# Kernel optimization log

Measured on AMD Instinct MI355X. Metric: run time of the kernel, lower is better.

## Reference

```python
import jax, jax.numpy as jnp
import numpy as np

B, I, H, NC, T = 128, 256, 512, 16, 24
M = 14            # max ACT ticks (forward default M=14)
EPS = 0.01        # eps_halting default


def setup_inputs() -> dict:
    key = jax.random.key(0)
    ks = jax.random.split(key, 9)
    s = 1.0 / np.sqrt(H).astype(np.float32)
    u = lambda k, shape: jax.random.uniform(k, shape, jnp.float32, -s, s)
    return {
        "x": jax.random.normal(ks[0], (B, I, T), jnp.float32),
        # LSTMCell params, torch gate order (i, f, g, o)
        "W_ih": u(ks[1], (4 * H, I)),
        "W_hh": u(ks[2], (4 * H, H)),
        "b_ih": u(ks[3], (4 * H,)),
        "b_hh": u(ks[4], (4 * H,)),
        "halt_w": u(ks[5], (1, H)),
        "halt_b": u(ks[6], (1,)),
        "dec_w": u(ks[7], (NC, H)),
        "dec_b": u(ks[8], (NC,)),
    }


def _forward(x, W_ih, W_hh, b_ih, b_hh, halt_w, halt_b, dec_w, dec_b):
    Bn = x.shape[0]
    Hn = W_hh.shape[1]

    def lstm_cell(xi, h, c):
        g = xi @ W_ih.T + b_ih + h @ W_hh.T + b_hh
        i, f, gg, o = jnp.split(g, 4, axis=-1)
        c = jax.nn.sigmoid(f) * c + jax.nn.sigmoid(i) * jnp.tanh(gg)
        h = jax.nn.sigmoid(o) * jnp.tanh(c)
        return h, c

    def act_step(carry, xi):
        # Run M ticks; ACT weighting (ph) zeroes contributions past the halt step,
        # exactly reproducing the torch early-exit semantics.
        def tick(sc, _):
            h, c = lstm_cell(xi, sc[0], sc[1])
            pn = jax.nn.sigmoid(h @ halt_w.T + halt_b)[:, 0]  # [B]
            y = h @ dec_w.T + dec_b                            # [B, NC]
            return (h, c), (pn, h, c, y)

        _, (p_hist, s_hist, c_hist, y_hist) = jax.lax.scan(tick, carry, None, length=M)
        # p_hist [M,B]; s/c_hist [M,B,H]; y_hist [M,B,NC]
        pt_cum = jnp.cumsum(p_hist, axis=0)                    # [M,B]
        all_halted = jnp.all(pt_cum >= 1.0 - EPS, axis=1)      # [M]
        n_stop = jnp.where(jnp.any(all_halted), jnp.argmax(all_halted) + 1, M)
        idx = jnp.arange(M)[:, None]
        # torch: p_max = min(1, cumsum); p_max[:, -1] = 1.0 (last executed tick)
        p_max = jnp.where(idx >= n_stop - 1, 1.0, jnp.minimum(1.0, pt_cum))
        ph = jnp.concatenate([p_max[:1], jnp.diff(p_max, axis=0)], axis=0)  # [M,B]
        st = jnp.einsum('mb,mbh->bh', ph, s_hist)
        ct = jnp.einsum('mb,mbh->bh', ph, c_hist)
        yt = jnp.einsum('mb,mbc->bc', ph, y_hist)
        nt = jnp.argmax(p_max, axis=0)                         # [B] first tick hitting 1.0
        rt = 1.0 - p_max[nt - 1, jnp.arange(Bn)]               # negative index wraps like torch
        pt = nt.astype(x.dtype) + rt
        return (st, ct), (yt, pt, nt)

    z = jnp.zeros((Bn, Hn), x.dtype)
    _, (Y, P, N) = jax.lax.scan(act_step, (z, z), jnp.moveaxis(x, -1, 0))
    Y = jnp.moveaxis(Y, 0, -1)     # [B, NC, T]
    P = jnp.sum(P, axis=0)         # [B]
    N = N.T                        # [B, T]
    return Y, P, N


def reference(x, W_ih, W_hh, b_ih, b_hh, halt_w, halt_b, dec_w, dec_b):
    return _forward(x, W_ih, W_hh, b_ih, b_hh, halt_w, halt_b, dec_w, dec_b)
```

## Files before the change

kernel.cpp:

```cpp
#include <hip/hip_runtime.h>
#include <math.h>

#define NWG 256
#define TPB 1024

static constexpr int Bc=128, Ic=256, Hc=512, NCc=16, Tc=24, Mc=14;
static constexpr int Y_SZ  = Bc*NCc*Tc;
static constexpr int P_OFF = Y_SZ;
static constexpr int N_OFF = Y_SZ + Bc;

static constexpr int HSZ    = Hc*Bc;
static constexpr int HB_OFF = 0;
static constexpr int SC_OFF = 2*HSZ;
static constexpr int HP_OFF = 4*HSZ;
static constexpr int DP_OFF = HP_OFF + 2*2048;

typedef float f4v __attribute__((ext_vector_type(4)));

__device__ __align__(64) unsigned g_bcnt[16][16];
__device__ __align__(64) unsigned g_bgen[16][16];
__device__ __align__(64) unsigned g_brc[16];
__device__ __align__(64) unsigned g_brg[16];

__device__ __forceinline__ float sigm(float v){ return 1.0f/(1.0f+expf(-v)); }

__device__ __forceinline__ void gstore(float* p, float v){
  __hip_atomic_store(p, v, __ATOMIC_RELAXED, __HIP_MEMORY_SCOPE_SYSTEM);
}
__device__ __forceinline__ float gload(const float* p){
  return *(const volatile float*)p;
}

__device__ __forceinline__ void gsync(int w){
  __syncthreads();
  if (threadIdx.x == 0) {
    asm volatile("" ::: "memory");
    const int g = w >> 4;
    unsigned prev = __hip_atomic_fetch_add(&g_bcnt[g][0], 1u, __ATOMIC_RELAXED, __HIP_MEMORY_SCOPE_SYSTEM);
    unsigned ep   = prev >> 4;
    if ((prev & 15u) == 15u) {
      unsigned rprev = __hip_atomic_fetch_add(&g_brc[0], 1u, __ATOMIC_RELAXED, __HIP_MEMORY_SCOPE_SYSTEM);
      if ((rprev & 15u) == 15u) {
        __hip_atomic_store(&g_brg[0], (rprev >> 4) + 1u, __ATOMIC_RELEASE, __HIP_MEMORY_SCOPE_SYSTEM);
      } else {
        while ((int)(__hip_atomic_load(&g_brg[0], __ATOMIC_RELAXED, __HIP_MEMORY_SCOPE_SYSTEM) - (ep + 1u)) < 0)
          __builtin_amdgcn_s_sleep(1);
      }
      __hip_atomic_store(&g_bgen[g][0], ep + 1u, __ATOMIC_RELEASE, __HIP_MEMORY_SCOPE_SYSTEM);
    } else {
      while ((int)(__hip_atomic_load(&g_bgen[g][0], __ATOMIC_RELAXED, __HIP_MEMORY_SCOPE_SYSTEM) - (ep + 1u)) < 0)
        __builtin_amdgcn_s_sleep(1);
    }
    asm volatile("" ::: "memory");
  }
  __syncthreads();
}

__global__ __launch_bounds__(TPB, 1) void act_lstm_kernel(
    const float* __restrict__ x,   const float* __restrict__ Wih,
    const float* __restrict__ Whh, const float* __restrict__ bih,
    const float* __restrict__ bhh, const float* __restrict__ hw,
    const float* __restrict__ hbp, const float* __restrict__ dw,
    const float* __restrict__ db,  float* __restrict__ out,
    float* __restrict__ ws)
{
  const int w    = blockIdx.x;
  const int tid  = threadIdx.x;
  const int lane = tid & 63;
  const int wid  = __builtin_amdgcn_readfirstlane(tid >> 6);
  const int bg   = w >> 4;
  const int js   = w & 15;
  const int kg   = wid;
  const int rl0  = lane, rl1 = lane + 64;
  const int grow0 = ((rl0>>5)<<9) + js*32 + (rl0&31);
  const int grow1 = ((rl1>>5)<<9) + js*32 + (rl1&31);
  const bool iscell = (tid < 256);
  const int jloc = tid >> 3, bl = tid & 7;
  const int jglob = js*32 + jloc;
  const int bglob = bg*8 + bl;

  float* hbuf = ws + HB_OFF;
  float* stc  = ws + SC_OFF;
  float* hpp  = ws + HP_OFF;
  float* decp = ws + DP_OFF;

  __shared__ float h_lds[4096];
  __shared__ float x_lds[2048];
  __shared__ float part[128*129];
  __shared__ float sums[1024];
  __shared__ float dp[4096];
  __shared__ float hp[256];
  __shared__ float pmh[128];
  __shared__ unsigned ldsu[2];

  const f4v* Wh0 = (const f4v*)(Whh + grow0*Hc) + kg*8;
  const f4v* Wh1 = (const f4v*)(Whh + grow1*Hc) + kg*8;
  const f4v* Wx0 = (const f4v*)(Wih + grow0*Ic) + kg*4;
  const f4v* Wx1 = (const f4v*)(Wih + grow1*Ic) + kg*4;

  float bsum[4] = {0,0,0,0};
  float hwj = 0.f;
  if (iscell) {
    #pragma unroll
    for (int g=0; g<4; ++g) bsum[g] = bih[g*512 + jglob] + bhh[g*512 + jglob];
    hwj = hw[jglob];
  }
  const float hb0 = hbp[0];

  float c = 0.f, st_run = 0.f, ct_run = 0.f, prev_pm = 0.f;
  float cumw=0.f, prevw=0.f, ntfw=0.f, rtvw=0.f, psumw=0.f;
  bool  ntsetw = false;
  int   gt = 0, lastpar = 0, pend_t = -1, pend_par = 0;
  float xg[4] = {0,0,0,0};

  for (int t = 0; t < Tc; ++t) {
    for (int mm = 0;; ++mm) {
      const bool do_h = !(mm == 0 && t == 0);
      float xv0 = 0.f, xv1 = 0.f;
      if (mm == 0) {
        const int i0 = tid >> 3, b0 = tid & 7;
        const int xb = (bg*8 + b0) * (Ic*Tc);
        xv0 = x[xb + i0*Tc + t];
        xv1 = x[xb + (i0+128)*Tc + t];
      }
      if (do_h) {
        const float* src = (mm == 0) ? (stc + lastpar*HSZ) : (hbuf + ((gt-1)&1)*HSZ);
        const int j = tid >> 1, q = tid & 1;
        f4v hv = *(const volatile f4v*)(src + j*128 + bg*8 + q*4);
        *(f4v*)&h_lds[tid*4] = hv;
      }
      __syncthreads();

      if (mm == 0) {
        x_lds[tid]        = xv0;
        x_lds[tid + 1024] = xv1;
        __syncthreads();
        float a0[8] = {0,0,0,0,0,0,0,0}, a1[8] = {0,0,0,0,0,0,0,0};
        #pragma unroll
        for (int c4 = 0; c4 < 4; ++c4) {
          f4v w0 = Wx0[c4], w1 = Wx1[c4];
          #pragma unroll
          for (int d = 0; d < 4; ++d) {
            const float wa = w0[d], wb = w1[d];
            const float* hbp_ = &x_lds[(kg*16 + c4*4 + d)*8];
            f4v hA = *(const f4v*)hbp_, hB = *(const f4v*)(hbp_+4);
            a0[0]=fmaf(wa,hA.x,a0[0]); a0[1]=fmaf(wa,hA.y,a0[1]);
            a0[2]=fmaf(wa,hA.z,a0[2]); a0[3]=fmaf(wa,hA.w,a0[3]);
            a0[4]=fmaf(wa,hB.x,a0[4]); a0[5]=fmaf(wa,hB.y,a0[5]);
            a0[6]=fmaf(wa,hB.z,a0[6]); a0[7]=fmaf(wa,hB.w,a0[7]);
            a1[0]=fmaf(wb,hA.x,a1[0]); a1[1]=fmaf(wb,hA.y,a1[1]);
            a1[2]=fmaf(wb,hA.z,a1[2]); a1[3]=fmaf(wb,hA.w,a1[3]);
            a1[4]=fmaf(wb,hB.x,a1[4]); a1[5]=fmaf(wb,hB.y,a1[5]);
            a1[6]=fmaf(wb,hB.z,a1[6]); a1[7]=fmaf(wb,hB.w,a1[7]);
          }
        }
        #pragma unroll
        for (int b = 0; b < 8; ++b) {
          part[rl0*129 + kg*8 + b] = a0[b];
          part[rl1*129 + kg*8 + b] = a1[b];
        }
        __syncthreads();
        {
          const int row = tid >> 3, b = tid & 7;
          float s = 0.f;
          #pragma unroll
          for (int q2 = 0; q2 < 16; ++q2) s += part[row*129 + q2*8 + b];
          sums[tid] = s;
        }
        __syncthreads();
        if (iscell) {
          #pragma unroll
          for (int g = 0; g < 4; ++g) xg[g] = bsum[g] + sums[(g*32 + jloc)*8 + bl];
        }
        __syncthreads();
      }

      {
        float a0[8] = {0,0,0,0,0,0,0,0}, a1[8] = {0,0,0,0,0,0,0,0};
        if (do_h) {
          #pragma unroll
          for (int c4 = 0; c4 < 8; ++c4) {
            f4v w0 = Wh0[c4], w1 = Wh1[c4];
            #pragma unroll
            for (int d = 0; d < 4; ++d) {
              const float wa = w0[d], wb = w1[d];
              const float* hbp_ = &h_lds[(kg*32 + c4*4 + d)*8];
              f4v hA = *(const f4v*)hbp_, hB = *(const f4v*)(hbp_+4);
              a0[0]=fmaf(wa,hA.x,a0[0]); a0[1]=fmaf(wa,hA.y,a0[1]);
              a0[2]=fmaf(wa,hA.z,a0[2]); a0[3]=fmaf(wa,hA.w,a0[3]);
              a0[4]=fmaf(wa,hB.x,a0[4]); a0[5]=fmaf(wa,hB.y,a0[5]);
              a0[6]=fmaf(wa,hB.z,a0[6]); a0[7]=fmaf(wa,hB.w,a0[7]);
              a1[0]=fmaf(wb,hA.x,a1[0]); a1[1]=fmaf(wb,hA.y,a1[1]);
              a1[2]=fmaf(wb,hA.z,a1[2]); a1[3]=fmaf(wb,hA.w,a1[3]);
              a1[4]=fmaf(wb,hB.x,a1[4]); a1[5]=fmaf(wb,hB.y,a1[5]);
              a1[6]=fmaf(wb,hB.z,a1[6]); a1[7]=fmaf(wb,hB.w,a1[7]);
            }
          }
        }
        #pragma unroll
        for (int b = 0; b < 8; ++b) {
          part[rl0*129 + kg*8 + b] = a0[b];
          part[rl1*129 + kg*8 + b] = a1[b];
        }
      }
      __syncthreads();
      {
        const int row = tid >> 3, b = tid & 7;
        float s = 0.f;
        #pragma unroll
        for (int q2 = 0; q2 < 16; ++q2) s += part[row*129 + q2*8 + b];
        sums[tid] = s;
      }
      __syncthreads();

      float hn = 0.f, cn = 0.f;
      if (iscell) {
        float g0 = xg[0] + sums[(0*32 + jloc)*8 + bl];
        float g1 = xg[1] + sums[(1*32 + jloc)*8 + bl];
        float g2 = xg[2] + sums[(2*32 + jloc)*8 + bl];
        float g3 = xg[3] + sums[(3*32 + jloc)*8 + bl];
        float ig = sigm(g0), fg = sigm(g1), gg = tanhf(g2), og = sigm(g3);
        cn = fg*c + ig*gg;
        hn = og*tanhf(cn);
        const int par = gt & 1;
        gstore(hbuf + par*HSZ + jglob*128 + bglob, hn);
        gstore(stc  + par*HSZ + jglob*128 + bglob, st_run + (1.f - prev_pm)*hn);
        hp[tid] = hn * hwj;
      }
      __syncthreads();
      if (tid < 8) {
        float s = 0.f;
        #pragma unroll
        for (int jl = 0; jl < 32; ++jl) s += hp[jl*8 + tid];
        gstore(hpp + (gt&1)*2048 + js*128 + bg*8 + tid, s);
      }

      gsync(w);

      if (pend_t >= 0) {
        if (js == 0 && tid < 128) {
          const int nc = tid >> 3, b2 = tid & 7;
          float y = 0.f;
          #pragma unroll
          for (int q2 = 0; q2 < 16; ++q2)
            y += gload(decp + pend_par*32768 + q2*2048 + nc*128 + bg*8 + b2);
          out[((bg*8 + b2)*NCc + nc)*Tc + pend_t] = y + db[nc];
        }
        pend_t = -1;
      }
      const int par = gt & 1;
      if (wid < 2) {
        const int b2 = wid*64 + lane;
        float hsum = 0.f;
        #pragma unroll
        for (int q2 = 0; q2 < 16; ++q2) hsum += gload(hpp + par*2048 + q2*128 + b2);
        float pn = sigm(hsum + hb0);
        cumw += pn;
        int ok = __all(cumw >= 0.99f) ? 1 : 0;
        if (lane == 0) ldsu[wid] = (unsigned)ok;
        pmh[b2] = fminf(1.f, cumw);
      }
      __syncthreads();
      const int finv = (((ldsu[0] & ldsu[1]) != 0u) || (mm == Mc-1)) ? 1 : 0;

      if (wid < 2) {
        float pmf = finv ? 1.f : fminf(1.f, cumw);
        if (!ntsetw && pmf >= 1.f) {
          ntfw = (float)mm;
          rtvw = (mm == 0) ? 0.f : (1.f - prevw);
          ntsetw = true;
        }
        prevw = pmf;
      }
      if (iscell) {
        float pm = finv ? 1.f : pmh[bglob];
        float ph = pm - prev_pm;
        st_run += ph*hn;
        ct_run += ph*cn;
        prev_pm = pm;
        c = finv ? ct_run : cn;
      }
      if (finv) {
        if (iscell) {
          #pragma unroll
          for (int nc = 0; nc < 16; ++nc)
            dp[nc*256 + tid] = dw[nc*512 + jglob] * st_run;
        }
        __syncthreads();
        if (tid < 128) {
          const int nc = tid >> 3, b2 = tid & 7;
          float s = 0.f;
          #pragma unroll
          for (int jl = 0; jl < 32; ++jl) s += dp[nc*256 + jl*8 + b2];
          gstore(decp + par*32768 + js*2048 + nc*128 + bg*8 + b2, s);
        }
        if (w == 0 && wid < 2)
          out[N_OFF + (wid*64 + lane)*Tc + t] = ntfw;
        if (wid < 2) {
          psumw += ntfw + rtvw;
          ntsetw = false; prevw = 0.f; cumw = 0.f; ntfw = 0.f; rtvw = 0.f;
        }
        if (iscell) { st_run = 0.f; ct_run = 0.f; prev_pm = 0.f; }
        pend_t = t; pend_par = par; lastpar = par;
      }
      ++gt;
      if (finv) break;
    }
  }

  gsync(w);
  if (pend_t >= 0 && js == 0 && tid < 128) {
    const int nc = tid >> 3, b2 = tid & 7;
    float y = 0.f;
    #pragma unroll
    for (int q2 = 0; q2 < 16; ++q2)
      y += gload(decp + pend_par*32768 + q2*2048 + nc*128 + bg*8 + b2);
    out[((bg*8 + b2)*NCc + nc)*Tc + pend_t] = y + db[nc];
  }
  if (w == 1 && wid < 2) out[P_OFF + wid*64 + lane] = psumw;
}

extern "C" void kernel_launch(void* const* d_in, const int* in_sizes, int n_in,
                              void* d_out, int out_size, void* d_ws, size_t ws_size,
                              hipStream_t stream) {
  const float* x   = (const float*)d_in[0];
  const float* Wih = (const float*)d_in[1];
  const float* Whh = (const float*)d_in[2];
  const float* bih = (const float*)d_in[3];
  const float* bhh = (const float*)d_in[4];
  const float* hw  = (const float*)d_in[5];
  const float* hb  = (const float*)d_in[6];
  const float* dwp = (const float*)d_in[7];
  const float* dbp = (const float*)d_in[8];
  float* out = (float*)d_out;
  float* ws  = (float*)d_ws;

  void* kargs[] = {(void*)&x, (void*)&Wih, (void*)&Whh, (void*)&bih, (void*)&bhh,
                   (void*)&hw, (void*)&hb, (void*)&dwp, (void*)&dbp, (void*)&out, (void*)&ws};
  hipLaunchCooperativeKernel((void*)act_lstm_kernel, dim3(NWG), dim3(TPB),
                             kargs, 0, stream);
}
```

Measured before the change: 2.178 ms.

## Retile work as 8 hidden units by 32 batch per block with 4x4 register tiles

Changes the work split from 32 hidden units by 8 batch rows per block to 8 hidden units by 32 batch rows. Each thread now computes a 4-row by 4-batch register tile, so every LDS h value it loads feeds more FMAs, and the partial-sum reduction is done in two halves to cut LDS use. The decoder output is now computed locally from the full gathered state at the next step instead of through a workspace partial-sum exchange. Each block must now gather 4x more h data and reduce 64 halting partials per tick, which adds global traffic and extra barriers.

```diff
diff --git a/kernel.cpp b/kernel.cpp
--- a/kernel.cpp
+++ b/kernel.cpp
@@ -13,7 +13,7 @@
 static constexpr int HB_OFF = 0;
 static constexpr int SC_OFF = 2*HSZ;
 static constexpr int HP_OFF = 4*HSZ;
-static constexpr int DP_OFF = HP_OFF + 2*2048;
+static constexpr int HPSZ   = 64*128;
 
 typedef float f4v __attribute__((ext_vector_type(4)));
 
@@ -26,9 +26,6 @@
 
 __device__ __forceinline__ void gstore(float* p, float v){
   __hip_atomic_store(p, v, __ATOMIC_RELAXED, __HIP_MEMORY_SCOPE_SYSTEM);
-}
-__device__ __forceinline__ float gload(const float* p){
-  return *(const volatile float*)p;
 }
 
 __device__ __forceinline__ void gsync(int w){
@@ -56,6 +53,38 @@
   __syncthreads();
 }
 
+#define TILE_FMA(s0,s1,s2,s3,hv)                                              \
+  a0.x=fmaf(s0,hv.x,a0.x); a0.y=fmaf(s0,hv.y,a0.y);                           \
+  a0.z=fmaf(s0,hv.z,a0.z); a0.w=fmaf(s0,hv.w,a0.w);                           \
+  a1.x=fmaf(s1,hv.x,a1.x); a1.y=fmaf(s1,hv.y,a1.y);                           \
+  a1.z=fmaf(s1,hv.z,a1.z); a1.w=fmaf(s1,hv.w,a1.w);                           \
+  a2.x=fmaf(s2,hv.x,a2.x); a2.y=fmaf(s2,hv.y,a2.y);                           \
+  a2.z=fmaf(s2,hv.z,a2.z); a2.w=fmaf(s2,hv.w,a2.w);                           \
+  a3.x=fmaf(s3,hv.x,a3.x); a3.y=fmaf(s3,hv.y,a3.y);                           \
+  a3.z=fmaf(s3,hv.z,a3.z); a3.w=fmaf(s3,hv.w,a3.w);
+
+#define WRITE_PART(q)                                                         \
+  *(f4v*)&part[(q)*1024 + (rgrp*4+0)*32 + b4*4] = a0;                         \
+  *(f4v*)&part[(q)*1024 + (rgrp*4+1)*32 + b4*4] = a1;                         \
+  *(f4v*)&part[(q)*1024 + (rgrp*4+2)*32 + b4*4] = a2;                         \
+  *(f4v*)&part[(q)*1024 + (rgrp*4+3)*32 + b4*4] = a3;
+
+#define REDUCE_TO_SUMS                                                        \
+  {                                                                           \
+    if (kg >= 8) { WRITE_PART(kg-8) }                                         \
+    __syncthreads();                                                          \
+    float racc = 0.f;                                                         \
+    _Pragma("unroll")                                                         \
+    for (int q=0;q<8;++q) racc += part[q*1024 + rr*32 + bb];                  \
+    __syncthreads();                                                          \
+    if (kg < 8) { WRITE_PART(kg) }                                            \
+    __syncthreads();                                                          \
+    _Pragma("unroll")                                                         \
+    for (int q=0;q<8;++q) racc += part[q*1024 + rr*32 + bb];                  \
+    sums[rr*32 + bb] = racc;                                                  \
+    __syncthreads();                                                          \
+  }
+
 __global__ __launch_bounds__(TPB, 1) void act_lstm_kernel(
     const float* __restrict__ x,   const float* __restrict__ Wih,
     const float* __restrict__ Whh, const float* __restrict__ bih,
@@ -68,211 +97,200 @@
   const int tid  = threadIdx.x;
   const int lane = tid & 63;
   const int wid  = __builtin_amdgcn_readfirstlane(tid >> 6);
-  const int bg   = w >> 4;
-  const int js   = w & 15;
+  const int jg   = w >> 2;
+  const int bgr  = w & 3;
+  const int rgrp = lane >> 3;
+  const int b4   = lane & 7;
   const int kg   = wid;
-  const int rl0  = lane, rl1 = lane + 64;
-  const int grow0 = ((rl0>>5)<<9) + js*32 + (rl0&31);
-  const int grow1 = ((rl1>>5)<<9) + js*32 + (rl1&31);
+  const int rr   = tid >> 5, bb = tid & 31;
   const bool iscell = (tid < 256);
-  const int jloc = tid >> 3, bl = tid & 7;
-  const int jglob = js*32 + jloc;
-  const int bglob = bg*8 + bl;
+  const int jloc = tid >> 5, bl = tid & 31;
+  const int jglob = jg*8 + jloc, bglob = bgr*32 + bl;
 
   float* hbuf = ws + HB_OFF;
   float* stc  = ws + SC_OFF;
   float* hpp  = ws + HP_OFF;
-  float* decp = ws + DP_OFF;
-
-  __shared__ float h_lds[4096];
-  __shared__ float x_lds[2048];
-  __shared__ float part[128*129];
+
+  __shared__ float h_lds[16384];
+  __shared__ float x_lds[8192];
+  __shared__ float part[8192];
   __shared__ float sums[1024];
-  __shared__ float dp[4096];
   __shared__ float hp[256];
+  __shared__ float hq2[512];
+  __shared__ float pnl[128];
   __shared__ float pmh[128];
   __shared__ unsigned ldsu[2];
-
-  const f4v* Wh0 = (const f4v*)(Whh + grow0*Hc) + kg*8;
-  const f4v* Wh1 = (const f4v*)(Whh + grow1*Hc) + kg*8;
-  const f4v* Wx0 = (const f4v*)(Wih + grow0*Ic) + kg*4;
-  const f4v* Wx1 = (const f4v*)(Wih + grow1*Ic) + kg*4;
-
+  float* hq = part;
+
+  const f4v* whr[4]; const f4v* wxr[4];
+  #pragma unroll
+  for (int i=0;i<4;++i){
+    int r = rgrp*4+i;
+    int grow = (r>>3)*512 + jg*8 + (r&7);
+    whr[i] = (const f4v*)(Whh + grow*Hc) + kg*8;
+    wxr[i] = (const f4v*)(Wih + grow*Ic) + kg*4;
+  }
   float bsum[4] = {0,0,0,0};
   float hwj = 0.f;
-  if (iscell) {
+  if (iscell){
     #pragma unroll
-    for (int g=0; g<4; ++g) bsum[g] = bih[g*512 + jglob] + bhh[g*512 + jglob];
+    for (int g=0;g<4;++g) bsum[g] = bih[g*512 + jglob] + bhh[g*512 + jglob];
     hwj = hw[jglob];
   }
   const float hb0 = hbp[0];
 
-  float c = 0.f, st_run = 0.f, ct_run = 0.f, prev_pm = 0.f;
+  float c=0.f, st_run=0.f, ct_run=0.f, prev_pm=0.f;
   float cumw=0.f, prevw=0.f, ntfw=0.f, rtvw=0.f, psumw=0.f;
-  bool  ntsetw = false;
-  int   gt = 0, lastpar = 0, pend_t = -1, pend_par = 0;
+  bool  ntsetw=false;
+  int   gt=0, lastpar=0;
   float xg[4] = {0,0,0,0};
 
-  for (int t = 0; t < Tc; ++t) {
-    for (int mm = 0;; ++mm) {
-      const bool do_h = !(mm == 0 && t == 0);
-      float xv0 = 0.f, xv1 = 0.f;
-      if (mm == 0) {
-        const int i0 = tid >> 3, b0 = tid & 7;
-        const int xb = (bg*8 + b0) * (Ic*Tc);
-        xv0 = x[xb + i0*Tc + t];
-        xv1 = x[xb + (i0+128)*Tc + t];
-      }
-      if (do_h) {
-        const float* src = (mm == 0) ? (stc + lastpar*HSZ) : (hbuf + ((gt-1)&1)*HSZ);
-        const int j = tid >> 1, q = tid & 1;
-        f4v hv = *(const volatile f4v*)(src + j*128 + bg*8 + q*4);
-        *(f4v*)&h_lds[tid*4] = hv;
-      }
-      __syncthreads();
-
-      if (mm == 0) {
-        x_lds[tid]        = xv0;
-        x_lds[tid + 1024] = xv1;
+  for (int t=0; t<Tc; ++t){
+    for (int mm=0;; ++mm){
+      const bool do_h = !(mm==0 && t==0);
+
+      if (mm == 0){
+        #pragma unroll
+        for (int u=0;u<8;++u){
+          int idx = u*1024 + tid, i = idx>>5, b2 = idx&31;
+          x_lds[idx] = x[(bgr*32 + b2)*(Ic*Tc) + i*Tc + t];
+        }
+        if (t > 0){
+          const float* src = stc + lastpar*HSZ;
+          #pragma unroll
+          for (int u=0;u<4;++u){
+            int f = u*1024 + tid, k = f>>3, q = f&7;
+            f4v hv = *(const volatile f4v*)(src + k*128 + bgr*32 + q*4);
+            *(f4v*)&h_lds[k*32 + q*4] = hv;
+          }
+        }
+      } else {
+        const float* src = hbuf + ((gt-1)&1)*HSZ;
+        #pragma unroll
+        for (int u=0;u<4;++u){
+          int f = u*1024 + tid, k = f>>3, q = f&7;
+          f4v hv = *(const volatile f4v*)(src + k*128 + bgr*32 + q*4);
+          *(f4v*)&h_lds[k*32 + q*4] = hv;
+        }
+      }
+      __syncthreads();
+
+      if (mm == 0){
+        f4v a0={0,0,0,0}, a1=a0, a2=a0, a3=a0;
+        #pragma unroll
+        for (int c4=0;c4<4;++c4){
+          f4v w0=wxr[0][c4], w1=wxr[1][c4], w2=wxr[2][c4], w3=wxr[3][c4];
+          #pragma unroll
+          for (int d=0;d<4;++d){
+            int ii = kg*16 + c4*4 + d;
+            f4v hv = *(const f4v*)&x_lds[ii*32 + b4*4];
+            TILE_FMA(w0[d], w1[d], w2[d], w3[d], hv)
+          }
+        }
+        REDUCE_TO_SUMS
+        if (iscell){
+          #pragma unroll
+          for (int g=0;g<4;++g) xg[g] = bsum[g] + sums[(g*8+jloc)*32 + bl];
+        }
         __syncthreads();
-        float a0[8] = {0,0,0,0,0,0,0,0}, a1[8] = {0,0,0,0,0,0,0,0};
-        #pragma unroll
-        for (int c4 = 0; c4 < 4; ++c4) {
-          f4v w0 = Wx0[c4], w1 = Wx1[c4];
-          #pragma unroll
-          for (int d = 0; d < 4; ++d) {
-            const float wa = w0[d], wb = w1[d];
-            const float* hbp_ = &x_lds[(kg*16 + c4*4 + d)*8];
-            f4v hA = *(const f4v*)hbp_, hB = *(const f4v*)(hbp_+4);
-            a0[0]=fmaf(wa,hA.x,a0[0]); a0[1]=fmaf(wa,hA.y,a0[1]);
-            a0[2]=fmaf(wa,hA.z,a0[2]); a0[3]=fmaf(wa,hA.w,a0[3]);
-            a0[4]=fmaf(wa,hB.x,a0[4]); a0[5]=fmaf(wa,hB.y,a0[5]);
-            a0[6]=fmaf(wa,hB.z,a0[6]); a0[7]=fmaf(wa,hB.w,a0[7]);
-            a1[0]=fmaf(wb,hA.x,a1[0]); a1[1]=fmaf(wb,hA.y,a1[1]);
-            a1[2]=fmaf(wb,hA.z,a1[2]); a1[3]=fmaf(wb,hA.w,a1[3]);
-            a1[4]=fmaf(wb,hB.x,a1[4]); a1[5]=fmaf(wb,hB.y,a1[5]);
-            a1[6]=fmaf(wb,hB.z,a1[6]); a1[7]=fmaf(wb,hB.w,a1[7]);
+        if (t > 0 && tid < 512){
+          int nc = tid>>5, b2 = tid&31;
+          float y = 0.f;
+          const f4v* dr = (const f4v*)(dw + nc*512);
+          #pragma unroll 4
+          for (int k4=0;k4<128;++k4){
+            f4v dv = dr[k4];
+            y = fmaf(dv.x, h_lds[(k4*4+0)*32 + b2], y);
+            y = fmaf(dv.y, h_lds[(k4*4+1)*32 + b2], y);
+            y = fmaf(dv.z, h_lds[(k4*4+2)*32 + b2], y);
+            y = fmaf(dv.w, h_lds[(k4*4+3)*32 + b2], y);
           }
-        }
-        #pragma unroll
-        for (int b = 0; b < 8; ++b) {
-          part[rl0*129 + kg*8 + b] = a0[b];
-          part[rl1*129 + kg*8 + b] = a1[b];
-        }
-        __syncthreads();
-        {
-          const int row = tid >> 3, b = tid & 7;
-          float s = 0.f;
-          #pragma unroll
-          for (int q2 = 0; q2 < 16; ++q2) s += part[row*129 + q2*8 + b];
-          sums[tid] = s;
-        }
-        __syncthreads();
-        if (iscell) {
-          #pragma unroll
-          for (int g = 0; g < 4; ++g) xg[g] = bsum[g] + sums[(g*32 + jloc)*8 + bl];
-        }
-        __syncthreads();
+          if (jg == 0) out[((bgr*32+b2)*NCc + nc)*Tc + (t-1)] = y + db[nc];
+        }
       }
 
       {
-        float a0[8] = {0,0,0,0,0,0,0,0}, a1[8] = {0,0,0,0,0,0,0,0};
-        if (do_h) {
-          #pragma unroll
-          for (int c4 = 0; c4 < 8; ++c4) {
-            f4v w0 = Wh0[c4], w1 = Wh1[c4];
+        f4v a0={0,0,0,0}, a1=a0, a2=a0, a3=a0;
+        if (do_h){
+          #pragma unroll
+          for (int c8=0;c8<8;++c8){
+            f4v w0=whr[0][c8], w1=whr[1][c8], w2=whr[2][c8], w3=whr[3][c8];
             #pragma unroll
-            for (int d = 0; d < 4; ++d) {
-              const float wa = w0[d], wb = w1[d];
-              const float* hbp_ = &h_lds[(kg*32 + c4*4 + d)*8];
-              f4v hA = *(const f4v*)hbp_, hB = *(const f4v*)(hbp_+4);
-              a0[0]=fmaf(wa,hA.x,a0[0]); a0[1]=fmaf(wa,hA.y,a0[1]);
-              a0[2]=fmaf(wa,hA.z,a0[2]); a0[3]=fmaf(wa,hA.w,a0[3]);
-              a0[4]=fmaf(wa,hB.x,a0[4]); a0[5]=fmaf(wa,hB.y,a0[5]);
-              a0[6]=fmaf(wa,hB.z,a0[6]); a0[7]=fmaf(wa,hB.w,a0[7]);
-              a1[0]=fmaf(wb,hA.x,a1[0]); a1[1]=fmaf(wb,hA.y,a1[1]);
-              a1[2]=fmaf(wb,hA.z,a1[2]); a1[3]=fmaf(wb,hA.w,a1[3]);
-              a1[4]=fmaf(wb,hB.x,a1[4]); a1[5]=fmaf(wb,hB.y,a1[5]);
-              a1[6]=fmaf(wb,hB.z,a1[6]); a1[7]=fmaf(wb,hB.w,a1[7]);
+            for (int d=0;d<4;++d){
+              int k = kg*32 + c8*4 + d;
+              f4v hv = *(const f4v*)&h_lds[k*32 + b4*4];
+              TILE_FMA(w0[d], w1[d], w2[d], w3[d], hv)
             }
           }
         }
-        #pragma unroll
-        for (int b = 0; b < 8; ++b) {
-          part[rl0*129 + kg*8 + b] = a0[b];
-          part[rl1*129 + kg*8 + b] = a1[b];
-        }
-      }
-      __syncthreads();
+        REDUCE_TO_SUMS
+      }
+
+      float hn=0.f, cn=0.f;
       {
-        const int row = tid >> 3, b = tid & 7;
+        const int par = gt & 1;
+        if (iscell){
+          float g0 = xg[0] + sums[(0*8+jloc)*32 + bl];
+          float g1 = xg[1] + sums[(1*8+jloc)*32 + bl];
+          float g2 = xg[2] + sums[(2*8+jloc)*32 + bl];
+          float g3 = xg[3] + sums[(3*8+jloc)*32 + bl];
+          float ig = sigm(g0), fg = sigm(g1), gg = tanhf(g2), og = sigm(g3);
+          cn = fg*c + ig*gg;
+          hn = og*tanhf(cn);
+          gstore(hbuf + par*HSZ + jglob*128 + bglob, hn);
+          gstore(stc  + par*HSZ + jglob*128 + bglob, st_run + (1.f - prev_pm)*hn);
+          hp[jloc*32 + bl] = hn * hwj;
+        }
+        __syncthreads();
+        if (tid < 32){
+          float s = 0.f;
+          #pragma unroll
+          for (int jl=0;jl<8;++jl) s += hp[jl*32 + tid];
+          gstore(hpp + par*HPSZ + jg*128 + bgr*32 + tid, s);
+        }
+      }
+
+      gsync(w);
+
+      {
+        const float* hpb = hpp + (gt&1)*HPSZ;
+        f4v q0 = *(const volatile f4v*)(hpb + tid*8);
+        f4v q1 = *(const volatile f4v*)(hpb + tid*8 + 4);
+        *(f4v*)&hq[tid*8]     = q0;
+        *(f4v*)&hq[tid*8 + 4] = q1;
+      }
+      __syncthreads();
+      if (tid < 512){
+        int q4 = tid >> 7, b2 = tid & 127;
         float s = 0.f;
-        #pragma unroll
-        for (int q2 = 0; q2 < 16; ++q2) s += part[row*129 + q2*8 + b];
-        sums[tid] = s;
-      }
-      __syncthreads();
-
-      float hn = 0.f, cn = 0.f;
-      if (iscell) {
-        float g0 = xg[0] + sums[(0*32 + jloc)*8 + bl];
-        float g1 = xg[1] + sums[(1*32 + jloc)*8 + bl];
-        float g2 = xg[2] + sums[(2*32 + jloc)*8 + bl];
-        float g3 = xg[3] + sums[(3*32 + jloc)*8 + bl];
-        float ig = sigm(g0), fg = sigm(g1), gg = tanhf(g2), og = sigm(g3);
-        cn = fg*c + ig*gg;
-        hn = og*tanhf(cn);
-        const int par = gt & 1;
-        gstore(hbuf + par*HSZ + jglob*128 + bglob, hn);
-        gstore(stc  + par*HSZ + jglob*128 + bglob, st_run + (1.f - prev_pm)*hn);
-        hp[tid] = hn * hwj;
-      }
-      __syncthreads();
-      if (tid < 8) {
-        float s = 0.f;
-        #pragma unroll
-        for (int jl = 0; jl < 32; ++jl) s += hp[jl*8 + tid];
-        gstore(hpp + (gt&1)*2048 + js*128 + bg*8 + tid, s);
-      }
-
-      gsync(w);
-
-      if (pend_t >= 0) {
-        if (js == 0 && tid < 128) {
-          const int nc = tid >> 3, b2 = tid & 7;
-          float y = 0.f;
-          #pragma unroll
-          for (int q2 = 0; q2 < 16; ++q2)
-            y += gload(decp + pend_par*32768 + q2*2048 + nc*128 + bg*8 + b2);
-          out[((bg*8 + b2)*NCc + nc)*Tc + pend_t] = y + db[nc];
-        }
-        pend_t = -1;
-      }
-      const int par = gt & 1;
-      if (wid < 2) {
-        const int b2 = wid*64 + lane;
-        float hsum = 0.f;
-        #pragma unroll
-        for (int q2 = 0; q2 < 16; ++q2) hsum += gload(hpp + par*2048 + q2*128 + b2);
-        float pn = sigm(hsum + hb0);
+        for (int j2 = q4*16; j2 < q4*16+16; ++j2) s += hq[j2*128 + b2];
+        hq2[q4*128 + b2] = s;
+      }
+      __syncthreads();
+      if (tid < 128)
+        pnl[tid] = (hq2[tid] + hq2[128+tid]) + (hq2[256+tid] + hq2[384+tid]);
+      __syncthreads();
+      if (wid < 2){
+        int btr = wid*64 + lane;
+        float pn = sigm(pnl[btr] + hb0);
         cumw += pn;
         int ok = __all(cumw >= 0.99f) ? 1 : 0;
         if (lane == 0) ldsu[wid] = (unsigned)ok;
-        pmh[b2] = fminf(1.f, cumw);
+        pmh[btr] = fminf(1.f, cumw);
       }
       __syncthreads();
       const int finv = (((ldsu[0] & ldsu[1]) != 0u) || (mm == Mc-1)) ? 1 : 0;
 
-      if (wid < 2) {
+      if (wid < 2){
         float pmf = finv ? 1.f : fminf(1.f, cumw);
-        if (!ntsetw && pmf >= 1.f) {
+        if (!ntsetw && pmf >= 1.f){
           ntfw = (float)mm;
           rtvw = (mm == 0) ? 0.f : (1.f - prevw);
           ntsetw = true;
         }
         prevw = pmf;
       }
-      if (iscell) {
+      if (iscell){
         float pm = finv ? 1.f : pmh[bglob];
         float ph = pm - prev_pm;
         st_run += ph*hn;
@@ -280,42 +298,44 @@
         prev_pm = pm;
         c = finv ? ct_run : cn;
       }
-      if (finv) {
-        if (iscell) {
-          #pragma unroll
-          for (int nc = 0; nc < 16; ++nc)
-            dp[nc*256 + tid] = dw[nc*512 + jglob] * st_run;
-        }
-        __syncthreads();
-        if (tid < 128) {
-          const int nc = tid >> 3, b2 = tid & 7;
-          float s = 0.f;
-          #pragma unroll
-          for (int jl = 0; jl < 32; ++jl) s += dp[nc*256 + jl*8 + b2];
-          gstore(decp + par*32768 + js*2048 + nc*128 + bg*8 + b2, s);
-        }
-        if (w == 0 && wid < 2)
-          out[N_OFF + (wid*64 + lane)*Tc + t] = ntfw;
-        if (wid < 2) {
+      if (finv){
+        if (w == 0 && wid < 2) out[N_OFF + (wid*64+lane)*Tc + t] = ntfw;
+        if (wid < 2){
           psumw += ntfw + rtvw;
-          ntsetw = false; prevw = 0.f; cumw = 0.f; ntfw = 0.f; rtvw = 0.f;
-        }
-        if (iscell) { st_run = 0.f; ct_run = 0.f; prev_pm = 0.f; }
-        pend_t = t; pend_par = par; lastpar = par;
+          ntsetw=false; prevw=0.f; cumw=0.f; ntfw=0.f; rtvw=0.f;
+        }
+        if (iscell){ st_run=0.f; ct_run=0.f; prev_pm=0.f; }
+        lastpar = gt & 1;
+        ++gt;
+        break;
       }
       ++gt;
-      if (finv) break;
     }
   }
 
-  gsync(w);
-  if (pend_t >= 0 && js == 0 && tid < 128) {
-    const int nc = tid >> 3, b2 = tid & 7;
-    float y = 0.f;
+  if (jg == 0){
+    const float* src = stc + lastpar*HSZ;
     #pragma unroll
-    for (int q2 = 0; q2 < 16; ++q2)
-      y += gload(decp + pend_par*32768 + q2*2048 + nc*128 + bg*8 + b2);
-    out[((bg*8 + b2)*NCc + nc)*Tc + pend_t] = y + db[nc];
+    for (int u=0;u<4;++u){
+      int f = u*1024 + tid, k = f>>3, q = f&7;
+      f4v hv = *(const volatile f4v*)(src + k*128 + bgr*32 + q*4);
+      *(f4v*)&h_lds[k*32 + q*4] = hv;
+    }
+    __syncthreads();
+    if (tid < 512){
+      int nc = tid>>5, b2 = tid&31;
+      float y = 0.f;
+      const f4v* dr = (const f4v*)(dw + nc*512);
+      #pragma unroll 4
+      for (int k4=0;k4<128;++k4){
+        f4v dv = dr[k4];
+        y = fmaf(dv.x, h_lds[(k4*4+0)*32 + b2], y);
+        y = fmaf(dv.y, h_lds[(k4*4+1)*32 + b2], y);
+        y = fmaf(dv.z, h_lds[(k4*4+2)*32 + b2], y);
+        y = fmaf(dv.w, h_lds[(k4*4+3)*32 + b2], y);
+      }
+      out[((bgr*32+b2)*NCc + nc)*Tc + (Tc-1)] = y + db[nc];
+    }
   }
   if (w == 1 && wid < 2) out[P_OFF + wid*64 + lane] = psumw;
 }
```

Result: slower. 2.356 ms (+8.2%).
